# Optimization experiments

Hardware: AMD Instinct MI355X
Metric: run time of the kernel (lower is better)

## Reference

```python
import jax, jax.numpy as jnp
import numpy as np

B, SQ, SK = 8, 128, 128
IVD, DIM, EV, H, NH = 32, 32, 64, 8, 128
DK = EV // H


def setup_inputs() -> dict:
    key = jax.random.key(0)
    ks = jax.random.split(key, 16)
    n = lambda k, s: jax.random.normal(k, s, dtype=jnp.float32)
    lin = lambda k, fi, fo: n(k, (fi, fo)) / np.float32(np.sqrt(fi))
    d = {}
    d['query_value'] = n(ks[0], (B, SQ, IVD))
    d['key_value']   = n(ks[1], (B, SK, IVD))
    d['value']       = n(ks[2], (B, SK, DIM))
    d['impute_data'] = n(ks[3], (B, SQ, IVD // 2))
    d['emb_mask'] = jax.random.randint(ks[4], (B, SK, DIM), 0, 2).astype(jnp.int32)
    # learn_value_embedding: Linear(IVD,NH)+Tanh+Linear(NH,EV,no bias)
    d['w1'] = lin(ks[5], IVD, NH); d['b1'] = jnp.zeros((NH,), jnp.float32)
    d['w2'] = lin(ks[6], NH, EV)
    # linears[0], linears[1]: Linear(EV,EV)
    d['wq'] = lin(ks[7], EV, EV); d['bq'] = jnp.zeros((EV,), jnp.float32)
    d['wk'] = lin(ks[8], EV, EV); d['bk'] = jnp.zeros((EV,), jnp.float32)
    # linears[2]: Linear(DIM*H, NH)
    d['wo'] = lin(ks[9], DIM * H, NH); d['bo'] = jnp.zeros((NH,), jnp.float32)
    # query_data_enc: Linear(IVD/2,NH)+LayerNorm(NH)+ReLU+Linear(NH,NH)
    d['wd1'] = lin(ks[10], IVD // 2, NH); d['bd1'] = jnp.zeros((NH,), jnp.float32)
    d['ln_g'] = jnp.ones((NH,), jnp.float32); d['ln_b'] = jnp.zeros((NH,), jnp.float32)
    d['wd2'] = lin(ks[11], NH, NH); d['bd2'] = jnp.zeros((NH,), jnp.float32)
    return d


def reference(query_value, key_value, value, impute_data,
              w1, b1, w2, wq, bq, wk, bk, wo, bo,
              wd1, bd1, ln_g, ln_b, wd2, bd2, emb_mask):
    b = query_value.shape[0]
    dim = value.shape[-1]
    # value embeddings: Linear -> Tanh -> Linear(no bias)
    qe = jnp.tanh(query_value @ w1 + b1) @ w2   # [B,Sq,EV]
    ke = jnp.tanh(key_value @ w1 + b1) @ w2     # [B,Sk,EV]
    q = (qe @ wq + bq).reshape(b, -1, H, DK).transpose(0, 2, 1, 3)  # [B,H,Sq,DK]
    k = (ke @ wk + bk).reshape(b, -1, H, DK).transpose(0, 2, 1, 3)  # [B,H,Sk,DK]
    scores = jnp.einsum('bhqd,bhkd->bhqk', q, k) / np.float32(np.sqrt(DK))
    # broadcast scores over the value channel dim; masked_fill with -10000
    m = emb_mask[:, None, None, :, :]           # [B,1,1,Sk,dim]
    logits = jnp.where(m == 0, jnp.float32(-10000.0), scores[..., None])  # [B,H,Sq,Sk,dim]
    p_attn = jax.nn.softmax(logits, axis=-2)    # softmax over Sk per channel
    out = jnp.einsum('bhqkd,bkd->bhqd', p_attn, value)  # [B,H,Sq,dim]
    x = out.transpose(0, 2, 1, 3).reshape(b, -1, H * dim)
    y = x @ wo + bo                             # [B,Sq,NH]
    # query_data_enc branch
    h1 = impute_data @ wd1 + bd1
    mu = jnp.mean(h1, axis=-1, keepdims=True)
    var = jnp.var(h1, axis=-1, keepdims=True)
    ln = (h1 - mu) / jnp.sqrt(var + 1e-5) * ln_g + ln_b
    query_data = jax.nn.relu(ln) @ wd2 + bd2    # [B,Sq,NH]
    return y, query_data
```

## Files before the change

kernel.cpp:

```cpp
#include <hip/hip_runtime.h>
#include <math.h>

#define B 8
#define SQ 128
#define SK 128
#define IVD 32
#define DIM 32
#define EV 64
#define H 8
#define NH 128
#define DK 8
#define TQ 2
#define KG 8

__device__ __forceinline__ float fast_tanh(float x) {
    const float xc = fminf(fmaxf(x, -10.f), 10.f);
    const float t = __expf(2.f * xc);
    return (t - 1.f) / (t + 1.f);
}

__global__ __launch_bounds__(128) void fused1_kernel(
    const float* __restrict__ qv, const float* __restrict__ kv,
    const float* __restrict__ w1, const float* __restrict__ b1,
    const float* __restrict__ w2,
    const float* __restrict__ wq, const float* __restrict__ bqv,
    const float* __restrict__ wk, const float* __restrict__ bkv,
    float* __restrict__ qout, float* __restrict__ kout,
    const float* __restrict__ imp,
    const float* __restrict__ wd1, const float* __restrict__ bd1,
    const float* __restrict__ ln_g, const float* __restrict__ ln_b,
    const float* __restrict__ wd2, const float* __restrict__ bd2,
    float* __restrict__ qd)
{
    const int r = blockIdx.x;
    const int tid = threadIdx.x;

    if (r < 1024) {
        __shared__ float xs[2][IVD];
        __shared__ float h1[2][NH];
        __shared__ float ev[2][EV];
        __shared__ float part[2][128];
        const float* src; const float* wp; const float* bp; float* dst;
        int row0;
        if (r < 512) { row0 = r * 2;         src = qv; wp = wq; bp = bqv; dst = qout; }
        else         { row0 = (r - 512) * 2; src = kv; wp = wk; bp = bkv; dst = kout; }

        if (tid < 2 * IVD) xs[tid >> 5][tid & 31] = src[row0 * IVD + tid];
        __syncthreads();

        {
            float a0 = b1[tid], a1 = a0;
            #pragma unroll
            for (int i = 0; i < IVD; ++i) {
                const float w = w1[i * NH + tid];
                a0 += xs[0][i] * w; a1 += xs[1][i] * w;
            }
            h1[0][tid] = fast_tanh(a0);
            h1[1][tid] = fast_tanh(a1);
        }
        __syncthreads();

        const int o = tid & 63, hf = tid >> 6;
        {
            float c0 = 0.f, c1 = 0.f;
            #pragma unroll 8
            for (int i = hf * 64; i < hf * 64 + 64; ++i) {
                const float w = w2[i * EV + o];
                c0 += h1[0][i] * w; c1 += h1[1][i] * w;
            }
            part[0][tid] = c0; part[1][tid] = c1;
        }
        __syncthreads();
        {
            const int row = tid >> 6, oo = tid & 63;
            ev[row][oo] = part[row][oo] + part[row][oo + 64];
        }
        __syncthreads();
        {
            float c0 = 0.f, c1 = 0.f;
            #pragma unroll 8
            for (int j = hf * 32; j < hf * 32 + 32; ++j) {
                const float w = wp[j * EV + o];
                c0 += ev[0][j] * w; c1 += ev[1][j] * w;
            }
            part[0][tid] = c0; part[1][tid] = c1;
        }
        __syncthreads();
        {
            const int row = tid >> 6, oo = tid & 63;
            dst[(row0 + row) * EV + oo] = part[row][oo] + part[row][oo + 64] + bp[oo];
        }
    } else {
        const int bs0 = (r - 1024) * 2;
        __shared__ float xs2[2][IVD / 2];
        __shared__ float h1b[2][NH];
        __shared__ float red[2][2];

        if (tid < IVD) xs2[tid >> 4][tid & 15] = imp[bs0 * (IVD / 2) + tid];
        __syncthreads();
        float a0 = bd1[tid], a1 = a0;
        #pragma unroll
        for (int i = 0; i < IVD / 2; ++i) {
            const float w = wd1[i * NH + tid];
            a0 += xs2[0][i] * w; a1 += xs2[1][i] * w;
        }

        float s0 = a0, s1 = a1;
        #pragma unroll
        for (int off = 32; off > 0; off >>= 1) {
            s0 += __shfl_down(s0, off, 64);
            s1 += __shfl_down(s1, off, 64);
        }
        if ((tid & 63) == 0) { red[0][tid >> 6] = s0; red[1][tid >> 6] = s1; }
        __syncthreads();
        const float mu0 = (red[0][0] + red[0][1]) * (1.f / NH);
        const float mu1 = (red[1][0] + red[1][1]) * (1.f / NH);
        const float d0 = a0 - mu0, d1 = a1 - mu1;
        float t0 = d0 * d0, t1 = d1 * d1;
        __syncthreads();
        #pragma unroll
        for (int off = 32; off > 0; off >>= 1) {
            t0 += __shfl_down(t0, off, 64);
            t1 += __shfl_down(t1, off, 64);
        }
        if ((tid & 63) == 0) { red[0][tid >> 6] = t0; red[1][tid >> 6] = t1; }
        __syncthreads();
        const float v0 = (red[0][0] + red[0][1]) * (1.f / NH);
        const float v1 = (red[1][0] + red[1][1]) * (1.f / NH);

        const float g = ln_g[tid], bb = ln_b[tid];
        h1b[0][tid] = fmaxf(d0 * rsqrtf(v0 + 1e-5f) * g + bb, 0.f);
        h1b[1][tid] = fmaxf(d1 * rsqrtf(v1 + 1e-5f) * g + bb, 0.f);
        __syncthreads();

        float c0 = bd2[tid], c1 = c0;
        #pragma unroll 8
        for (int j = 0; j < NH; ++j) {
            const float w = wd2[j * NH + tid];
            c0 += h1b[0][j] * w; c1 += h1b[1][j] * w;
        }
        qd[bs0 * NH + tid] = c0;
        qd[(bs0 + 1) * NH + tid] = c1;
    }
}

__global__ __launch_bounds__(512, 4) void attn_kernel(
    const float* __restrict__ qproj, const float* __restrict__ kproj,
    const float* __restrict__ value, const int* __restrict__ mask,
    const float* __restrict__ wo, const float* __restrict__ bo,
    float* __restrict__ y)
{
    const int blk = blockIdx.x;
    const int b = blk >> 6;
    const int q0 = (blk & 63) * TQ;
    const int tid = threadIdx.x;

    __shared__ __align__(16) float qs[TQ * EV];
    __shared__ __align__(16) float sc[TQ * H * SK];
    __shared__ __align__(16) float2 part[TQ * H * KG * DIM];
    __shared__ __align__(16) float xr[TQ * H * DIM];
    __shared__ __align__(16) float ypart[4][TQ * NH];

    const int d = tid & 31, kg = (tid >> 5) & 7, qh = tid >> 8;

    float4 vv[4], mq[4];
    {
        const float* vb = value + b * SK * DIM + d;
        const int*   mb = mask  + b * SK * DIM + d;
        #pragma unroll
        for (int j = 0; j < 4; ++j) {
            const int k0 = kg * 16 + j * 4;
            const float m0 = (float)mb[(k0 + 0) * DIM];
            const float m1 = (float)mb[(k0 + 1) * DIM];
            const float m2 = (float)mb[(k0 + 2) * DIM];
            const float m3 = (float)mb[(k0 + 3) * DIM];
            mq[j] = make_float4(m0, m1, m2, m3);
            vv[j] = make_float4(vb[(k0 + 0) * DIM] * m0,
                                vb[(k0 + 1) * DIM] * m1,
                                vb[(k0 + 2) * DIM] * m2,
                                vb[(k0 + 3) * DIM] * m3);
        }
    }

    if (tid < TQ * EV) qs[tid] = qproj[(b * SQ + q0) * EV + tid] * 0.3535533905932738f;
    __syncthreads();

    #pragma unroll
    for (int i = 0; i < (TQ * H * SK) / 512; ++i) {
        const int p = tid + i * 512;
        const int q = p >> 10, rem = p & 1023, h = rem >> 7, k = rem & 127;
        const float4* kr = (const float4*)(kproj + (b * SK + k) * EV + h * DK);
        const float4* qq = (const float4*)(qs + q * EV + h * DK);
        const float4 k0 = kr[0], k1 = kr[1], qa = qq[0], qb = qq[1];
        const float s = qa.x * k0.x + qa.y * k0.y + qa.z * k0.z + qa.w * k0.w
                      + qb.x * k1.x + qb.y * k1.y + qb.z * k1.z + qb.w * k1.w;
        sc[p] = __expf(s);
    }
    __syncthreads();

    #pragma unroll
    for (int h = 0; h < H; ++h) {
        const float4* sp = (const float4*)&sc[(qh * H + h) * SK + kg * 16];
        float num = 0.f, den = 0.f;
        #pragma unroll
        for (int j = 0; j < 4; ++j) {
            const float4 s = sp[j];
            num += s.x * vv[j].x + s.y * vv[j].y + s.z * vv[j].z + s.w * vv[j].w;
            den += s.x * mq[j].x + s.y * mq[j].y + s.z * mq[j].z + s.w * mq[j].w;
        }
        part[((qh * H + h) * KG + kg) * DIM + d] = make_float2(num, den);
    }
    __syncthreads();
    {
        const int h2 = (tid >> 5) & 7;
        float num = 0.f, den = 0.f;
        #pragma unroll
        for (int g = 0; g < KG; ++g) {
            const float2 p2 = part[((qh * H + h2) * KG + g) * DIM + d];
            num += p2.x; den += p2.y;
        }
        xr[qh * (H * DIM) + h2 * DIM + d] = num / den;
    }
    __syncthreads();

    {
        const int n = tid & 127, quarter = tid >> 7;
        const float* wop = wo + quarter * 64 * NH + n;
        const float* x0 = xr + quarter * 64;
        const float* x1 = xr + (H * DIM) + quarter * 64;
        float a0 = 0.f, a1 = 0.f;
        #pragma unroll 4
        for (int j = 0; j < 64; ++j) {
            const float w = wop[j * NH];
            a0 += w * x0[j];
            a1 += w * x1[j];
        }
        ypart[quarter][0 * NH + n] = a0;
        ypart[quarter][1 * NH + n] = a1;
    }
    __syncthreads();
    if (tid < TQ * NH) {
        const int q = tid >> 7, n = tid & 127;
        y[(b * SQ + q0 + q) * NH + n] =
            (ypart[0][q * NH + n] + ypart[1][q * NH + n])
          + (ypart[2][q * NH + n] + ypart[3][q * NH + n]) + bo[n];
    }
}

extern "C" void kernel_launch(void* const* d_in, const int* in_sizes, int n_in,
                              void* d_out, int out_size, void* d_ws, size_t ws_size,
                              hipStream_t stream) {
    const float* query_value = (const float*)d_in[0];
    const float* key_value   = (const float*)d_in[1];
    const float* value       = (const float*)d_in[2];
    const float* impute      = (const float*)d_in[3];
    const int*   emb_mask    = (const int*)d_in[4];
    const float* w1   = (const float*)d_in[5];
    const float* b1   = (const float*)d_in[6];
    const float* w2   = (const float*)d_in[7];
    const float* wq   = (const float*)d_in[8];
    const float* bq   = (const float*)d_in[9];
    const float* wk   = (const float*)d_in[10];
    const float* bk   = (const float*)d_in[11];
    const float* wo   = (const float*)d_in[12];
    const float* bo   = (const float*)d_in[13];
    const float* wd1  = (const float*)d_in[14];
    const float* bd1  = (const float*)d_in[15];
    const float* ln_g = (const float*)d_in[16];
    const float* ln_b = (const float*)d_in[17];
    const float* wd2  = (const float*)d_in[18];
    const float* bd2  = (const float*)d_in[19];

    float* y  = (float*)d_out;
    float* qd = y + B * SQ * NH;

    float* qproj = (float*)d_ws;
    float* kproj = qproj + B * SQ * EV;

    hipLaunchKernelGGL(fused1_kernel, dim3(1536), dim3(128), 0, stream,
                       query_value, key_value, w1, b1, w2, wq, bq, wk, bk,
                       qproj, kproj,
                       impute, wd1, bd1, ln_g, ln_b, wd2, bd2, qd);
    hipLaunchKernelGGL(attn_kernel, dim3(B * SQ / TQ), dim3(512), 0, stream,
                       qproj, kproj, value, emb_mask, wo, bo, y);
}
```

Before: 113.3 us.

## Move query-data encoder into attention kernel and prefetch attention inputs into cache

The impute/LayerNorm encoder branch moves from the first kernel into extra blocks of the attention kernel, each 512-thread block handling 8 rows with four 128-thread teams. This shortens the first kernel and fills idle CUs during the attention launch. The projection kernel also issues dummy loads of value, mask and wo so they sit in L2 before the attention kernel reads them. The cost is more shared memory per attention block, which could lower occupancy, plus extra memory traffic from the prefetch loads.

```diff
diff --git a/kernel.cpp b/kernel.cpp
--- a/kernel.cpp
+++ b/kernel.cpp
@@ -19,140 +19,93 @@
     return (t - 1.f) / (t + 1.f);
 }
 
-__global__ __launch_bounds__(128) void fused1_kernel(
+__global__ __launch_bounds__(128) void proj_kernel(
     const float* __restrict__ qv, const float* __restrict__ kv,
     const float* __restrict__ w1, const float* __restrict__ b1,
     const float* __restrict__ w2,
     const float* __restrict__ wq, const float* __restrict__ bqv,
     const float* __restrict__ wk, const float* __restrict__ bkv,
     float* __restrict__ qout, float* __restrict__ kout,
+    const float* __restrict__ value, const int* __restrict__ mask,
+    const float* __restrict__ wo)
+{
+    const int r = blockIdx.x;
+    const int tid = threadIdx.x;
+
+    {
+        const int g = r * 128 + tid;
+        if (g < 1024)      { const float v = value[g * 32];          asm volatile("" :: "v"(v)); }
+        else if (g < 2048) { const int   m = mask[(g - 1024) * 32];  asm volatile("" :: "v"(m)); }
+        else if (g < 3072) { const float w = wo[(g - 2048) * 32];    asm volatile("" :: "v"(w)); }
+    }
+
+    __shared__ float xs[2][IVD];
+    __shared__ float h1[2][NH];
+    __shared__ float ev[2][EV];
+    __shared__ float part[2][128];
+    const float* src; const float* wp; const float* bp; float* dst;
+    int row0;
+    if (r < 512) { row0 = r * 2;         src = qv; wp = wq; bp = bqv; dst = qout; }
+    else         { row0 = (r - 512) * 2; src = kv; wp = wk; bp = bkv; dst = kout; }
+
+    if (tid < 2 * IVD) xs[tid >> 5][tid & 31] = src[row0 * IVD + tid];
+    __syncthreads();
+
+    {
+        float a0 = b1[tid], a1 = a0;
+        #pragma unroll
+        for (int i = 0; i < IVD; ++i) {
+            const float w = w1[i * NH + tid];
+            a0 += xs[0][i] * w; a1 += xs[1][i] * w;
+        }
+        h1[0][tid] = fast_tanh(a0);
+        h1[1][tid] = fast_tanh(a1);
+    }
+    __syncthreads();
+
+    const int o = tid & 63, hf = tid >> 6;
+    {
+        float c0 = 0.f, c1 = 0.f;
+        #pragma unroll 8
+        for (int i = hf * 64; i < hf * 64 + 64; ++i) {
+            const float w = w2[i * EV + o];
+            c0 += h1[0][i] * w; c1 += h1[1][i] * w;
+        }
+        part[0][tid] = c0; part[1][tid] = c1;
+    }
+    __syncthreads();
+    {
+        const int row = tid >> 6, oo = tid & 63;
+        ev[row][oo] = part[row][oo] + part[row][oo + 64];
+    }
+    __syncthreads();
+    {
+        float c0 = 0.f, c1 = 0.f;
+        #pragma unroll 8
+        for (int j = hf * 32; j < hf * 32 + 32; ++j) {
+            const float w = wp[j * EV + o];
+            c0 += ev[0][j] * w; c1 += ev[1][j] * w;
+        }
+        part[0][tid] = c0; part[1][tid] = c1;
+    }
+    __syncthreads();
+    {
+        const int row = tid >> 6, oo = tid & 63;
+        dst[(row0 + row) * EV + oo] = part[row][oo] + part[row][oo + 64] + bp[oo];
+    }
+}
+
+__global__ __launch_bounds__(512, 4) void attn_kernel(
+    const float* __restrict__ qproj, const float* __restrict__ kproj,
+    const float* __restrict__ value, const int* __restrict__ mask,
+    const float* __restrict__ wo, const float* __restrict__ bo,
     const float* __restrict__ imp,
     const float* __restrict__ wd1, const float* __restrict__ bd1,
     const float* __restrict__ ln_g, const float* __restrict__ ln_b,
     const float* __restrict__ wd2, const float* __restrict__ bd2,
-    float* __restrict__ qd)
-{
-    const int r = blockIdx.x;
-    const int tid = threadIdx.x;
-
-    if (r < 1024) {
-        __shared__ float xs[2][IVD];
-        __shared__ float h1[2][NH];
-        __shared__ float ev[2][EV];
-        __shared__ float part[2][128];
-        const float* src; const float* wp; const float* bp; float* dst;
-        int row0;
-        if (r < 512) { row0 = r * 2;         src = qv; wp = wq; bp = bqv; dst = qout; }
-        else         { row0 = (r - 512) * 2; src = kv; wp = wk; bp = bkv; dst = kout; }
-
-        if (tid < 2 * IVD) xs[tid >> 5][tid & 31] = src[row0 * IVD + tid];
-        __syncthreads();
-
-        {
-            float a0 = b1[tid], a1 = a0;
-            #pragma unroll
-            for (int i = 0; i < IVD; ++i) {
-                const float w = w1[i * NH + tid];
-                a0 += xs[0][i] * w; a1 += xs[1][i] * w;
-            }
-            h1[0][tid] = fast_tanh(a0);
-            h1[1][tid] = fast_tanh(a1);
-        }
-        __syncthreads();
-
-        const int o = tid & 63, hf = tid >> 6;
-        {
-            float c0 = 0.f, c1 = 0.f;
-            #pragma unroll 8
-            for (int i = hf * 64; i < hf * 64 + 64; ++i) {
-                const float w = w2[i * EV + o];
-                c0 += h1[0][i] * w; c1 += h1[1][i] * w;
-            }
-            part[0][tid] = c0; part[1][tid] = c1;
-        }
-        __syncthreads();
-        {
-            const int row = tid >> 6, oo = tid & 63;
-            ev[row][oo] = part[row][oo] + part[row][oo + 64];
-        }
-        __syncthreads();
-        {
-            float c0 = 0.f, c1 = 0.f;
-            #pragma unroll 8
-            for (int j = hf * 32; j < hf * 32 + 32; ++j) {
-                const float w = wp[j * EV + o];
-                c0 += ev[0][j] * w; c1 += ev[1][j] * w;
-            }
-            part[0][tid] = c0; part[1][tid] = c1;
-        }
-        __syncthreads();
-        {
-            const int row = tid >> 6, oo = tid & 63;
-            dst[(row0 + row) * EV + oo] = part[row][oo] + part[row][oo + 64] + bp[oo];
-        }
-    } else {
-        const int bs0 = (r - 1024) * 2;
-        __shared__ float xs2[2][IVD / 2];
-        __shared__ float h1b[2][NH];
-        __shared__ float red[2][2];
-
-        if (tid < IVD) xs2[tid >> 4][tid & 15] = imp[bs0 * (IVD / 2) + tid];
-        __syncthreads();
-        float a0 = bd1[tid], a1 = a0;
-        #pragma unroll
-        for (int i = 0; i < IVD / 2; ++i) {
-            const float w = wd1[i * NH + tid];
-            a0 += xs2[0][i] * w; a1 += xs2[1][i] * w;
-        }
-
-        float s0 = a0, s1 = a1;
-        #pragma unroll
-        for (int off = 32; off > 0; off >>= 1) {
-            s0 += __shfl_down(s0, off, 64);
-            s1 += __shfl_down(s1, off, 64);
-        }
-        if ((tid & 63) == 0) { red[0][tid >> 6] = s0; red[1][tid >> 6] = s1; }
-        __syncthreads();
-        const float mu0 = (red[0][0] + red[0][1]) * (1.f / NH);
-        const float mu1 = (red[1][0] + red[1][1]) * (1.f / NH);
-        const float d0 = a0 - mu0, d1 = a1 - mu1;
-        float t0 = d0 * d0, t1 = d1 * d1;
-        __syncthreads();
-        #pragma unroll
-        for (int off = 32; off > 0; off >>= 1) {
-            t0 += __shfl_down(t0, off, 64);
-            t1 += __shfl_down(t1, off, 64);
-        }
-        if ((tid & 63) == 0) { red[0][tid >> 6] = t0; red[1][tid >> 6] = t1; }
-        __syncthreads();
-        const float v0 = (red[0][0] + red[0][1]) * (1.f / NH);
-        const float v1 = (red[1][0] + red[1][1]) * (1.f / NH);
-
-        const float g = ln_g[tid], bb = ln_b[tid];
-        h1b[0][tid] = fmaxf(d0 * rsqrtf(v0 + 1e-5f) * g + bb, 0.f);
-        h1b[1][tid] = fmaxf(d1 * rsqrtf(v1 + 1e-5f) * g + bb, 0.f);
-        __syncthreads();
-
-        float c0 = bd2[tid], c1 = c0;
-        #pragma unroll 8
-        for (int j = 0; j < NH; ++j) {
-            const float w = wd2[j * NH + tid];
-            c0 += h1b[0][j] * w; c1 += h1b[1][j] * w;
-        }
-        qd[bs0 * NH + tid] = c0;
-        qd[(bs0 + 1) * NH + tid] = c1;
-    }
-}
-
-__global__ __launch_bounds__(512, 4) void attn_kernel(
-    const float* __restrict__ qproj, const float* __restrict__ kproj,
-    const float* __restrict__ value, const int* __restrict__ mask,
-    const float* __restrict__ wo, const float* __restrict__ bo,
-    float* __restrict__ y)
+    float* __restrict__ y, float* __restrict__ qd)
 {
     const int blk = blockIdx.x;
-    const int b = blk >> 6;
-    const int q0 = (blk & 63) * TQ;
     const int tid = threadIdx.x;
 
     __shared__ __align__(16) float qs[TQ * EV];
@@ -160,90 +113,150 @@
     __shared__ __align__(16) float2 part[TQ * H * KG * DIM];
     __shared__ __align__(16) float xr[TQ * H * DIM];
     __shared__ __align__(16) float ypart[4][TQ * NH];
-
-    const int d = tid & 31, kg = (tid >> 5) & 7, qh = tid >> 8;
-
-    float4 vv[4], mq[4];
-    {
-        const float* vb = value + b * SK * DIM + d;
-        const int*   mb = mask  + b * SK * DIM + d;
-        #pragma unroll
-        for (int j = 0; j < 4; ++j) {
-            const int k0 = kg * 16 + j * 4;
-            const float m0 = (float)mb[(k0 + 0) * DIM];
-            const float m1 = (float)mb[(k0 + 1) * DIM];
-            const float m2 = (float)mb[(k0 + 2) * DIM];
-            const float m3 = (float)mb[(k0 + 3) * DIM];
-            mq[j] = make_float4(m0, m1, m2, m3);
-            vv[j] = make_float4(vb[(k0 + 0) * DIM] * m0,
-                                vb[(k0 + 1) * DIM] * m1,
-                                vb[(k0 + 2) * DIM] * m2,
-                                vb[(k0 + 3) * DIM] * m3);
-        }
-    }
-
-    if (tid < TQ * EV) qs[tid] = qproj[(b * SQ + q0) * EV + tid] * 0.3535533905932738f;
-    __syncthreads();
-
-    #pragma unroll
-    for (int i = 0; i < (TQ * H * SK) / 512; ++i) {
-        const int p = tid + i * 512;
-        const int q = p >> 10, rem = p & 1023, h = rem >> 7, k = rem & 127;
-        const float4* kr = (const float4*)(kproj + (b * SK + k) * EV + h * DK);
-        const float4* qq = (const float4*)(qs + q * EV + h * DK);
-        const float4 k0 = kr[0], k1 = kr[1], qa = qq[0], qb = qq[1];
-        const float s = qa.x * k0.x + qa.y * k0.y + qa.z * k0.z + qa.w * k0.w
-                      + qb.x * k1.x + qb.y * k1.y + qb.z * k1.z + qb.w * k1.w;
-        sc[p] = __expf(s);
-    }
-    __syncthreads();
-
-    #pragma unroll
-    for (int h = 0; h < H; ++h) {
-        const float4* sp = (const float4*)&sc[(qh * H + h) * SK + kg * 16];
-        float num = 0.f, den = 0.f;
-        #pragma unroll
-        for (int j = 0; j < 4; ++j) {
-            const float4 s = sp[j];
-            num += s.x * vv[j].x + s.y * vv[j].y + s.z * vv[j].z + s.w * vv[j].w;
-            den += s.x * mq[j].x + s.y * mq[j].y + s.z * mq[j].z + s.w * mq[j].w;
-        }
-        part[((qh * H + h) * KG + kg) * DIM + d] = make_float2(num, den);
-    }
-    __syncthreads();
-    {
-        const int h2 = (tid >> 5) & 7;
-        float num = 0.f, den = 0.f;
-        #pragma unroll
-        for (int g = 0; g < KG; ++g) {
-            const float2 p2 = part[((qh * H + h2) * KG + g) * DIM + d];
-            num += p2.x; den += p2.y;
-        }
-        xr[qh * (H * DIM) + h2 * DIM + d] = num / den;
-    }
-    __syncthreads();
-
-    {
-        const int n = tid & 127, quarter = tid >> 7;
-        const float* wop = wo + quarter * 64 * NH + n;
-        const float* x0 = xr + quarter * 64;
-        const float* x1 = xr + (H * DIM) + quarter * 64;
-        float a0 = 0.f, a1 = 0.f;
-        #pragma unroll 4
-        for (int j = 0; j < 64; ++j) {
-            const float w = wop[j * NH];
-            a0 += w * x0[j];
-            a1 += w * x1[j];
-        }
-        ypart[quarter][0 * NH + n] = a0;
-        ypart[quarter][1 * NH + n] = a1;
-    }
-    __syncthreads();
-    if (tid < TQ * NH) {
-        const int q = tid >> 7, n = tid & 127;
-        y[(b * SQ + q0 + q) * NH + n] =
-            (ypart[0][q * NH + n] + ypart[1][q * NH + n])
-          + (ypart[2][q * NH + n] + ypart[3][q * NH + n]) + bo[n];
+    __shared__ float xs2[4][2][IVD / 2];
+    __shared__ float h1b[4][2][NH];
+    __shared__ float red[4][2][2];
+
+    if (blk < 512) {
+        const int b = blk >> 6;
+        const int q0 = (blk & 63) * TQ;
+
+        const int d = tid & 31, kg = (tid >> 5) & 7, qh = tid >> 8;
+
+        float4 vv[4], mq[4];
+        {
+            const float* vb = value + b * SK * DIM + d;
+            const int*   mb = mask  + b * SK * DIM + d;
+            #pragma unroll
+            for (int j = 0; j < 4; ++j) {
+                const int k0 = kg * 16 + j * 4;
+                const float m0 = (float)mb[(k0 + 0) * DIM];
+                const float m1 = (float)mb[(k0 + 1) * DIM];
+                const float m2 = (float)mb[(k0 + 2) * DIM];
+                const float m3 = (float)mb[(k0 + 3) * DIM];
+                mq[j] = make_float4(m0, m1, m2, m3);
+                vv[j] = make_float4(vb[(k0 + 0) * DIM] * m0,
+                                    vb[(k0 + 1) * DIM] * m1,
+                                    vb[(k0 + 2) * DIM] * m2,
+                                    vb[(k0 + 3) * DIM] * m3);
+            }
+        }
+
+        if (tid < TQ * EV)
+            qs[tid] = qproj[(b * SQ + q0) * EV + tid] * 0.3535533905932738f;
+        __syncthreads();
+
+        #pragma unroll
+        for (int i = 0; i < (TQ * H * SK) / 512; ++i) {
+            const int p = tid + i * 512;
+            const int q = p >> 10, rem = p & 1023, h = rem >> 7, k = rem & 127;
+            const float4* kr = (const float4*)(kproj + (b * SK + k) * EV + h * DK);
+            const float4* qq = (const float4*)(qs + q * EV + h * DK);
+            const float4 k0 = kr[0], k1 = kr[1], qa = qq[0], qb = qq[1];
+            const float s = qa.x * k0.x + qa.y * k0.y + qa.z * k0.z + qa.w * k0.w
+                          + qb.x * k1.x + qb.y * k1.y + qb.z * k1.z + qb.w * k1.w;
+            sc[p] = __expf(s);
+        }
+        __syncthreads();
+
+        #pragma unroll
+        for (int h = 0; h < H; ++h) {
+            const float4* sp = (const float4*)&sc[(qh * H + h) * SK + kg * 16];
+            float num = 0.f, den = 0.f;
+            #pragma unroll
+            for (int j = 0; j < 4; ++j) {
+                const float4 s = sp[j];
+                num += s.x * vv[j].x + s.y * vv[j].y + s.z * vv[j].z + s.w * vv[j].w;
+                den += s.x * mq[j].x + s.y * mq[j].y + s.z * mq[j].z + s.w * mq[j].w;
+            }
+            part[((qh * H + h) * KG + kg) * DIM + d] = make_float2(num, den);
+        }
+        __syncthreads();
+        {
+            const int h2 = (tid >> 5) & 7;
+            float num = 0.f, den = 0.f;
+            #pragma unroll
+            for (int g = 0; g < KG; ++g) {
+                const float2 p2 = part[((qh * H + h2) * KG + g) * DIM + d];
+                num += p2.x; den += p2.y;
+            }
+            xr[qh * (H * DIM) + h2 * DIM + d] = num / den;
+        }
+        __syncthreads();
+
+        {
+            const int n = tid & 127, quarter = tid >> 7;
+            const float* wop = wo + quarter * 64 * NH + n;
+            const float* x0 = xr + quarter * 64;
+            const float* x1 = xr + (H * DIM) + quarter * 64;
+            float a0 = 0.f, a1 = 0.f;
+            #pragma unroll 4
+            for (int j = 0; j < 64; ++j) {
+                const float w = wop[j * NH];
+                a0 += w * x0[j];
+                a1 += w * x1[j];
+            }
+            ypart[quarter][0 * NH + n] = a0;
+            ypart[quarter][1 * NH + n] = a1;
+        }
+        __syncthreads();
+        if (tid < TQ * NH) {
+            const int q = tid >> 7, n = tid & 127;
+            y[(b * SQ + q0 + q) * NH + n] =
+                (ypart[0][q * NH + n] + ypart[1][q * NH + n])
+              + (ypart[2][q * NH + n] + ypart[3][q * NH + n]) + bo[n];
+        }
+    } else {
+        const int ib = blk - 512;
+        const int team = tid >> 7;
+        const int t = tid & 127;
+        const int bs0 = ib * 8 + team * 2;
+
+        if (t < IVD) xs2[team][t >> 4][t & 15] = imp[bs0 * (IVD / 2) + t];
+        __syncthreads();
+        float a0 = bd1[t], a1 = a0;
+        #pragma unroll
+        for (int i = 0; i < IVD / 2; ++i) {
+            const float w = wd1[i * NH + t];
+            a0 += xs2[team][0][i] * w; a1 += xs2[team][1][i] * w;
+        }
+
+        float s0 = a0, s1 = a1;
+        #pragma unroll
+        for (int off = 32; off > 0; off >>= 1) {
+            s0 += __shfl_down(s0, off, 64);
+            s1 += __shfl_down(s1, off, 64);
+        }
+        if ((t & 63) == 0) { red[team][0][t >> 6] = s0; red[team][1][t >> 6] = s1; }
+        __syncthreads();
+        const float mu0 = (red[team][0][0] + red[team][0][1]) * (1.f / NH);
+        const float mu1 = (red[team][1][0] + red[team][1][1]) * (1.f / NH);
+        const float d0 = a0 - mu0, d1 = a1 - mu1;
+        float t0 = d0 * d0, t1 = d1 * d1;
+        __syncthreads();
+        #pragma unroll
+        for (int off = 32; off > 0; off >>= 1) {
+            t0 += __shfl_down(t0, off, 64);
+            t1 += __shfl_down(t1, off, 64);
+        }
+        if ((t & 63) == 0) { red[team][0][t >> 6] = t0; red[team][1][t >> 6] = t1; }
+        __syncthreads();
+        const float v0 = (red[team][0][0] + red[team][0][1]) * (1.f / NH);
+        const float v1 = (red[team][1][0] + red[team][1][1]) * (1.f / NH);
+
+        const float g = ln_g[t], bb = ln_b[t];
+        h1b[team][0][t] = fmaxf(d0 * rsqrtf(v0 + 1e-5f) * g + bb, 0.f);
+        h1b[team][1][t] = fmaxf(d1 * rsqrtf(v1 + 1e-5f) * g + bb, 0.f);
+        __syncthreads();
+
+        float c0 = bd2[t], c1 = c0;
+        #pragma unroll 8
+        for (int j = 0; j < NH; ++j) {
+            const float w = wd2[j * NH + t];
+            c0 += h1b[team][0][j] * w; c1 += h1b[team][1][j] * w;
+        }
+        qd[bs0 * NH + t] = c0;
+        qd[(bs0 + 1) * NH + t] = c1;
     }
 }
 
@@ -277,10 +290,10 @@
     float* qproj = (float*)d_ws;
     float* kproj = qproj + B * SQ * EV;
 
-    hipLaunchKernelGGL(fused1_kernel, dim3(1536), dim3(128), 0, stream,
+    hipLaunchKernelGGL(proj_kernel, dim3(1024), dim3(128), 0, stream,
                        query_value, key_value, w1, b1, w2, wq, bq, wk, bk,
-                       qproj, kproj,
-                       impute, wd1, bd1, ln_g, ln_b, wd2, bd2, qd);
-    hipLaunchKernelGGL(attn_kernel, dim3(B * SQ / TQ), dim3(512), 0, stream,
-                       qproj, kproj, value, emb_mask, wo, bo, y);
-}
+                       qproj, kproj, value, emb_mask, wo);
+    hipLaunchKernelGGL(attn_kernel, dim3(512 + 128), dim3(512), 0, stream,
+                       qproj, kproj, value, emb_mask, wo, bo,
+                       impute, wd1, bd1, ln_g, ln_b, wd2, bd2, y, qd);
+}
```

New measurement: 114.0 us. About the same (+0.6%).
